# Kernel tuning notes

Measured on AMD Instinct MI355X. Metric: run time of the kernel, lower is better.

## Reference

```python
import jax, jax.numpy as jnp
import numpy as np

B, C, Q, H = 32, 2048, 512, 1024

def setup_inputs() -> dict:
    key = jax.random.key(0)
    k1, k2 = jax.random.split(key)
    similarity = jax.random.normal(k1, (B, C, Q), dtype=jnp.float32)
    qencode = jax.random.normal(k2, (B, Q, H), dtype=jnp.float32)
    return {"similarity": similarity, "qencode": qencode}

def reference(similarity, qencode):
    # softmax over query axis, then weighted sum of query encodings:
    # equivalent to the expand_dims*multiply*reduce_sum in the original,
    # expressed as a fused softmax + batched matmul.
    attn = jax.nn.softmax(similarity, axis=-1)          # [B, C, Q]
    return jnp.einsum('bcq,bqh->bch', attn, qencode)    # [B, C, H]
```

## Files before the change

### kernel.cpp

```cpp
#include <hip/hip_runtime.h>
#include <hip/hip_bf16.h>

typedef unsigned short ushort_t;
typedef __bf16 bf16x8 __attribute__((ext_vector_type(8)));
typedef float f32x4 __attribute__((ext_vector_type(4)));

#define B_  32
#define C_  2048
#define Q_  512
#define H_  1024

__device__ __forceinline__ unsigned short f2bf(float f) {
  unsigned u = __float_as_uint(f);
  u += 0x7FFFu + ((u >> 16) & 1u);
  return (unsigned short)(u >> 16);
}

__global__ __launch_bounds__(256) void softmax_bf16(const float* __restrict__ sim,
                                                    ushort_t* __restrict__ attn) {
  const int row  = (blockIdx.x << 2) | (threadIdx.x >> 6);
  const int lane = threadIdx.x & 63;
  const float4* rp = reinterpret_cast<const float4*>(sim + (size_t)row * Q_);
  float4 v0 = rp[lane];
  float4 v1 = rp[64 + lane];
  float x[8] = {v0.x, v0.y, v0.z, v0.w, v1.x, v1.y, v1.z, v1.w};

  float mx = x[0];
#pragma unroll
  for (int j = 1; j < 8; ++j) mx = fmaxf(mx, x[j]);
#pragma unroll
  for (int s = 32; s > 0; s >>= 1) mx = fmaxf(mx, __shfl_xor(mx, s, 64));

  float e[8], sum = 0.f;
#pragma unroll
  for (int j = 0; j < 8; ++j) { e[j] = __expf(x[j] - mx); sum += e[j]; }
#pragma unroll
  for (int s = 32; s > 0; s >>= 1) sum += __shfl_xor(sum, s, 64);
  const float inv = 1.0f / sum;

  union { ushort_t s[4]; uint2 v; } a, b;
#pragma unroll
  for (int j = 0; j < 4; ++j) {
    a.s[j] = f2bf(e[j] * inv);
    b.s[j] = f2bf(e[4 + j] * inv);
  }
  ushort_t* orow = attn + (size_t)row * Q_;
  *reinterpret_cast<uint2*>(orow + lane * 4)       = a.v;
  *reinterpret_cast<uint2*>(orow + 256 + lane * 4) = b.v;
}

__global__ __launch_bounds__(256) void qenc_convert(const float* __restrict__ qe,
                                                    ushort_t* __restrict__ qt) {
  __shared__ float tile[64][65];
  const int b  = blockIdx.z;
  const int q0 = blockIdx.y << 6;
  const int h0 = blockIdx.x << 6;

  const float* src = qe + ((size_t)b * Q_ + q0) * H_ + h0;
#pragma unroll
  for (int i = 0; i < 4; ++i) {
    const int idx = i * 256 + threadIdx.x;
    const int r  = idx >> 4;
    const int c4 = (idx & 15) << 2;
    const float4 v = *reinterpret_cast<const float4*>(src + (size_t)r * H_ + c4);
    tile[r][c4 + 0] = v.x;
    tile[r][c4 + 1] = v.y;
    tile[r][c4 + 2] = v.z;
    tile[r][c4 + 3] = v.w;
  }
  __syncthreads();

  const int hh = threadIdx.x >> 2;
  const int qs = (threadIdx.x & 3) << 4;
  ushort_t* dst = qt + ((size_t)b * H_ + h0 + hh) * Q_ + q0 + qs;

  union { ushort_t s[8]; uint4 v; } ha, hb;
#pragma unroll
  for (int j = 0; j < 8; ++j) {
    ha.s[j] = f2bf(tile[qs + j][hh]);
    hb.s[j] = f2bf(tile[qs + 8 + j][hh]);
  }
  *reinterpret_cast<uint4*>(dst)     = ha.v;
  *reinterpret_cast<uint4*>(dst + 8) = hb.v;
}

__global__ __launch_bounds__(256) void gemm_bt(const ushort_t* __restrict__ A,
                                               const ushort_t* __restrict__ Bt,
                                               float* __restrict__ out) {
  constexpr int BK = 64;
  __shared__ ushort_t As[128 * BK];
  __shared__ ushort_t Bs[128 * BK];

  const int id = blockIdx.x;
  const int sw = (id & 7) * 512 + (id >> 3);
  const int b   = sw >> 7;
  const int rem = sw & 127;
  const int c0 = (rem >> 3) << 7;
  const int h0 = (rem & 7) << 7;

  const int t    = threadIdx.x;
  const int lane = t & 63;
  const int w    = t >> 6;
  const int wm = (w >> 1) << 6;
  const int wn = (w & 1) << 6;

  const ushort_t* Ab = A  + (size_t)b * C_ * Q_;
  const ushort_t* Bb = Bt + (size_t)b * H_ * Q_;

  f32x4 acc[4][4];
#pragma unroll
  for (int m = 0; m < 4; ++m)
#pragma unroll
    for (int n = 0; n < 4; ++n) acc[m][n] = (f32x4){0.f, 0.f, 0.f, 0.f};

  const int fr = lane & 15;
  const int fk = (lane >> 4) * 8;

  for (int kt = 0; kt < 8; ++kt) {
    const int kOff = kt * BK;

    __syncthreads();
#pragma unroll
    for (int i = 0; i < 4; ++i) {
      const int idd = i * 256 + t;
      const int r = idd >> 3, cch = (idd & 7) << 3;
      __builtin_amdgcn_global_load_lds(
          (const __attribute__((address_space(1))) unsigned*)(Ab + (size_t)(c0 + r) * Q_ + kOff + cch),
          (__attribute__((address_space(3))) unsigned*)(As + idd * 8), 16, 0, 0);
    }
#pragma unroll
    for (int i = 0; i < 4; ++i) {
      const int idd = i * 256 + t;
      const int r = idd >> 3, cch = (idd & 7) << 3;
      __builtin_amdgcn_global_load_lds(
          (const __attribute__((address_space(1))) unsigned*)(Bb + (size_t)(h0 + r) * Q_ + kOff + cch),
          (__attribute__((address_space(3))) unsigned*)(Bs + idd * 8), 16, 0, 0);
    }
    asm volatile("s_waitcnt vmcnt(0)" ::: "memory");
    __syncthreads();

#pragma unroll
    for (int ks = 0; ks < 2; ++ks) {
      const int ko = ks * 32 + fk;
      bf16x8 af[4], bfr[4];
#pragma unroll
      for (int m = 0; m < 4; ++m)
        af[m] = *reinterpret_cast<const bf16x8*>(&As[(wm + m * 16 + fr) * BK + ko]);
#pragma unroll
      for (int n = 0; n < 4; ++n)
        bfr[n] = *reinterpret_cast<const bf16x8*>(&Bs[(wn + n * 16 + fr) * BK + ko]);
#pragma unroll
      for (int m = 0; m < 4; ++m)
#pragma unroll
        for (int n = 0; n < 4; ++n)
          acc[m][n] = __builtin_amdgcn_mfma_f32_16x16x32_bf16(af[m], bfr[n], acc[m][n], 0, 0, 0);
    }
  }

  float* ob = out + (size_t)b * C_ * H_;
  const int orow = c0 + wm + ((lane >> 4) << 2);
  const int ocol = h0 + wn + fr;
#pragma unroll
  for (int m = 0; m < 4; ++m)
#pragma unroll
    for (int n = 0; n < 4; ++n) {
#pragma unroll
      for (int j = 0; j < 4; ++j)
        ob[(size_t)(orow + m * 16 + j) * H_ + (ocol + n * 16)] = acc[m][n][j];
    }
}

extern "C" void kernel_launch(void* const* d_in, const int* in_sizes, int n_in,
                              void* d_out, int out_size, void* d_ws, size_t ws_size,
                              hipStream_t stream) {
  const float* sim  = (const float*)d_in[0];
  const float* qenc = (const float*)d_in[1];
  float* out = (float*)d_out;

  ushort_t* attn = (ushort_t*)d_ws;
  ushort_t* qt   = (ushort_t*)((char*)d_ws + (size_t)B_ * C_ * Q_ * sizeof(ushort_t));

  softmax_bf16<<<(B_ * C_) / 4, 256, 0, stream>>>(sim, attn);
  qenc_convert<<<dim3(H_ / 64, Q_ / 64, B_), 256, 0, stream>>>(qenc, qt);
  gemm_bt<<<4096, 256, 0, stream>>>(attn, qt, out);
}
```

Before: 518.2 us.

## Enlarge GEMM tiles to 256x256 with 512 threads and double-buffer LDS

The batched GEMM moves from 128x128 tiles on 256 threads to 256x256 tiles on 512 threads (8 waves, each computing a 128x64 sub-tile). LDS staging is double-buffered so the next K slice loads while MFMAs run on the current one, and one barrier per iteration is removed. The goal is more operand reuse, fewer redundant global reads and hidden load latency. The cost is 128 KB of LDS and 128 accumulator registers per thread, which lowers occupancy and leaves only 1024 blocks.

```diff
diff --git a/kernel.cpp b/kernel.cpp
--- a/kernel.cpp
+++ b/kernel.cpp
@@ -84,84 +84,87 @@
   *reinterpret_cast<uint4*>(dst + 8) = hb.v;
 }
 
-__global__ __launch_bounds__(256) void gemm_bt(const ushort_t* __restrict__ A,
+__global__ __launch_bounds__(512) void gemm_bt(const ushort_t* __restrict__ A,
                                                const ushort_t* __restrict__ Bt,
                                                float* __restrict__ out) {
   constexpr int BK = 64;
-  __shared__ ushort_t As[128 * BK];
-  __shared__ ushort_t Bs[128 * BK];
+  __shared__ ushort_t As[2][256 * BK];
+  __shared__ ushort_t Bs[2][256 * BK];
 
   const int id = blockIdx.x;
-  const int sw = (id & 7) * 512 + (id >> 3);
-  const int b   = sw >> 7;
-  const int rem = sw & 127;
-  const int c0 = (rem >> 3) << 7;
-  const int h0 = (rem & 7) << 7;
+  const int sw = (id & 7) * 128 + (id >> 3);
+  const int b   = sw >> 5;
+  const int rem = sw & 31;
+  const int c0 = (rem >> 2) << 8;
+  const int h0 = (rem & 3) << 8;
 
   const int t    = threadIdx.x;
   const int lane = t & 63;
   const int w    = t >> 6;
-  const int wm = (w >> 1) << 6;
-  const int wn = (w & 1) << 6;
+  const int wm = (w >> 2) << 7;
+  const int wn = (w & 3) << 6;
 
   const ushort_t* Ab = A  + (size_t)b * C_ * Q_;
   const ushort_t* Bb = Bt + (size_t)b * H_ * Q_;
 
-  f32x4 acc[4][4];
+  f32x4 acc[8][4];
 #pragma unroll
-  for (int m = 0; m < 4; ++m)
+  for (int m = 0; m < 8; ++m)
 #pragma unroll
     for (int n = 0; n < 4; ++n) acc[m][n] = (f32x4){0.f, 0.f, 0.f, 0.f};
 
   const int fr = lane & 15;
   const int fk = (lane >> 4) * 8;
 
-  for (int kt = 0; kt < 8; ++kt) {
-    const int kOff = kt * BK;
-
-    __syncthreads();
+  auto stage = [&](int buf, int kOff) {
 #pragma unroll
     for (int i = 0; i < 4; ++i) {
-      const int idd = i * 256 + t;
-      const int r = idd >> 3, cch = (idd & 7) << 3;
+      const int idd = i * 512 + t;
+      const int r = idd >> 3, cc = (idd & 7) << 3;
       __builtin_amdgcn_global_load_lds(
-          (const __attribute__((address_space(1))) unsigned*)(Ab + (size_t)(c0 + r) * Q_ + kOff + cch),
-          (__attribute__((address_space(3))) unsigned*)(As + idd * 8), 16, 0, 0);
+          (const __attribute__((address_space(1))) unsigned*)(Ab + (size_t)(c0 + r) * Q_ + kOff + cc),
+          (__attribute__((address_space(3))) unsigned*)(&As[buf][idd * 8]), 16, 0, 0);
+      __builtin_amdgcn_global_load_lds(
+          (const __attribute__((address_space(1))) unsigned*)(Bb + (size_t)(h0 + r) * Q_ + kOff + cc),
+          (__attribute__((address_space(3))) unsigned*)(&Bs[buf][idd * 8]), 16, 0, 0);
     }
-#pragma unroll
-    for (int i = 0; i < 4; ++i) {
-      const int idd = i * 256 + t;
-      const int r = idd >> 3, cch = (idd & 7) << 3;
-      __builtin_amdgcn_global_load_lds(
-          (const __attribute__((address_space(1))) unsigned*)(Bb + (size_t)(h0 + r) * Q_ + kOff + cch),
-          (__attribute__((address_space(3))) unsigned*)(Bs + idd * 8), 16, 0, 0);
-    }
-    asm volatile("s_waitcnt vmcnt(0)" ::: "memory");
-    __syncthreads();
+  };
+
+  stage(0, 0);
+  asm volatile("s_waitcnt vmcnt(0)" ::: "memory");
+  __syncthreads();
+
+  int cur = 0;
+  for (int kt = 0; kt < 8; ++kt) {
+    if (kt < 7) stage(cur ^ 1, (kt + 1) * BK);
 
 #pragma unroll
     for (int ks = 0; ks < 2; ++ks) {
       const int ko = ks * 32 + fk;
-      bf16x8 af[4], bfr[4];
+      bf16x8 af[8], bfr[4];
 #pragma unroll
-      for (int m = 0; m < 4; ++m)
-        af[m] = *reinterpret_cast<const bf16x8*>(&As[(wm + m * 16 + fr) * BK + ko]);
+      for (int m = 0; m < 8; ++m)
+        af[m] = *reinterpret_cast<const bf16x8*>(&As[cur][(wm + m * 16 + fr) * BK + ko]);
 #pragma unroll
       for (int n = 0; n < 4; ++n)
-        bfr[n] = *reinterpret_cast<const bf16x8*>(&Bs[(wn + n * 16 + fr) * BK + ko]);
+        bfr[n] = *reinterpret_cast<const bf16x8*>(&Bs[cur][(wn + n * 16 + fr) * BK + ko]);
 #pragma unroll
-      for (int m = 0; m < 4; ++m)
+      for (int m = 0; m < 8; ++m)
 #pragma unroll
         for (int n = 0; n < 4; ++n)
           acc[m][n] = __builtin_amdgcn_mfma_f32_16x16x32_bf16(af[m], bfr[n], acc[m][n], 0, 0, 0);
     }
+
+    asm volatile("s_waitcnt vmcnt(0)" ::: "memory");
+    __syncthreads();
+    cur ^= 1;
   }
 
   float* ob = out + (size_t)b * C_ * H_;
   const int orow = c0 + wm + ((lane >> 4) << 2);
   const int ocol = h0 + wn + fr;
 #pragma unroll
-  for (int m = 0; m < 4; ++m)
+  for (int m = 0; m < 8; ++m)
 #pragma unroll
     for (int n = 0; n < 4; ++n) {
 #pragma unroll
@@ -182,5 +185,5 @@
 
   softmax_bf16<<<(B_ * C_) / 4, 256, 0, stream>>>(sim, attn);
   qenc_convert<<<dim3(H_ / 64, Q_ / 64, B_), 256, 0, stream>>>(qenc, qt);
-  gemm_bt<<<4096, 256, 0, stream>>>(attn, qt, out);
+  gemm_bt<<<1024, 512, 0, stream>>>(attn, qt, out);
 }
```

Result: faster. 491.8 us (-5.1%).
